# Optimization experiments

Hardware: AMD Instinct MI355X
Metric: run time of the kernel (lower is better)

The kernel has to match this reference:

```python
import jax, jax.numpy as jnp
import numpy as np

N = 10000
E = 320000
IN_CH = 256
OUT4 = 256  # 4 * out_channels, out_channels = 64


def setup_inputs() -> dict:
    key = jax.random.key(0)
    k1, k2, k3 = jax.random.split(key, 3)
    x = jax.random.normal(k1, (N, IN_CH), dtype=jnp.float32)
    edge_index = jax.random.randint(k2, (2, E), 0, N, dtype=jnp.int64)
    stdv = 1.0 / np.sqrt(64.0)  # 1/sqrt(out_channels), as in __init__
    weight = jax.random.uniform(k3, (IN_CH, OUT4), dtype=jnp.float32,
                                minval=-stdv, maxval=stdv)
    return {"x": x, "weight": weight, "edge_index": edge_index}


def reference(x, weight, edge_index):
    n = x.shape[0]
    idx = jnp.arange(n)
    # dense adjacency with self-loops (duplicates/edges just set to 1)
    adj = jnp.zeros((n, n), dtype=x.dtype)
    adj = adj.at[idx, idx].set(1.0)
    adj = adj.at[edge_index[0], edge_index[1]].set(1.0)
    # symmetric degree normalization D^-1/2 A D^-1/2
    deg = jnp.sum(adj, axis=1)  # >= 1 due to self-loops
    d_inv_sqrt = jax.lax.rsqrt(deg)
    norm_adj = adj * d_inv_sqrt[:, None] * d_inv_sqrt[None, :]
    # aggregate then project: (A_norm @ x) @ W
    return jnp.matmul(jnp.matmul(norm_adj, x), weight)
```

## Files before the change

kernel.cpp:

```cpp
#include <hip/hip_runtime.h>


#define CH 256
#define ELLW 96
#define FB 80
#define RPB 125

typedef __attribute__((ext_vector_type(8))) short short8;
typedef __attribute__((ext_vector_type(4))) float f32x4;

__device__ inline unsigned short f2b(float f) {
    unsigned x = __builtin_bit_cast(unsigned, f);
    x = (x + 0x7fffu + ((x >> 16) & 1u)) >> 16;
    return (unsigned short)x;
}
__device__ inline float b2f(unsigned short u) {
    unsigned v = ((unsigned)u) << 16;
    return __builtin_bit_cast(float, v);
}

__global__ void prep_kernel(const float* __restrict__ w,
                            unsigned short* __restrict__ wt) {
    int idx = blockIdx.x * blockDim.x + threadIdx.x;
    if (idx < CH * CH) {
        int k = idx >> 8, nn = idx & 255;
        wt[nn * CH + k] = f2b(w[idx]);
    }
}

__global__ __launch_bounds__(1024) void fillgemm_kernel(
    const int* __restrict__ ei, int e_cnt, int* __restrict__ cnt,
    int* __restrict__ col_ell,
    const float* __restrict__ x, const unsigned short* __restrict__ wt,
    unsigned short* __restrict__ zb, int n) {
    __shared__ int lcnt[RPB];
    if ((int)blockIdx.x < FB) {
        const int lo = blockIdx.x * RPB;
        for (int i = threadIdx.x; i < RPB; i += 1024) lcnt[i] = 0;
        __syncthreads();
        const int4* r4 = (const int4*)ei;
        const int4* c4 = (const int4*)(ei + e_cnt);
        const int n4 = e_cnt >> 2;
        for (int i = threadIdx.x; i < n4; i += 1024) {
            int4 rv = r4[i];
            int4 cv = c4[i];
            int d0 = rv.x - lo, d1 = rv.y - lo, d2 = rv.z - lo, d3 = rv.w - lo;
            if ((unsigned)d0 < RPB) {
                int pos = atomicAdd(&lcnt[d0], 1);
                if (pos < ELLW) col_ell[(size_t)rv.x * ELLW + pos] = cv.x;
            }
            if ((unsigned)d1 < RPB) {
                int pos = atomicAdd(&lcnt[d1], 1);
                if (pos < ELLW) col_ell[(size_t)rv.y * ELLW + pos] = cv.y;
            }
            if ((unsigned)d2 < RPB) {
                int pos = atomicAdd(&lcnt[d2], 1);
                if (pos < ELLW) col_ell[(size_t)rv.z * ELLW + pos] = cv.z;
            }
            if ((unsigned)d3 < RPB) {
                int pos = atomicAdd(&lcnt[d3], 1);
                if (pos < ELLW) col_ell[(size_t)rv.w * ELLW + pos] = cv.w;
            }
        }
        __syncthreads();
        for (int i = threadIdx.x; i < RPB; i += 1024) cnt[lo + i] = lcnt[i];
        return;
    }
    const int blk = blockIdx.x - FB;
    const int tid = threadIdx.x;
    const int lane = tid & 63;
    const int wv = tid >> 6;
    const int m0 = blk * 64 + (wv >> 2) * 16;
    if (m0 >= n) return;
    const int n0 = (wv & 3) * 64;
    const int rsel = lane & 15;
    const int kbase = (lane >> 4) * 8;

    const float* xrow = x + (size_t)(m0 + rsel) * CH + kbase;
    const unsigned short* b0p = wt + (size_t)(n0 + rsel) * CH + kbase;
    const unsigned short* b1p = b0p + 16 * CH;
    const unsigned short* b2p = b0p + 32 * CH;
    const unsigned short* b3p = b0p + 48 * CH;

    f32x4 acc0 = {0.f, 0.f, 0.f, 0.f};
    f32x4 acc1 = acc0, acc2 = acc0, acc3 = acc0;

#pragma unroll
    for (int kc = 0; kc < 8; ++kc) {
        const float4* p = (const float4*)(xrow + kc * 32);
        float4 u = p[0], v = p[1];
        short8 a;
        a[0] = (short)f2b(u.x); a[1] = (short)f2b(u.y);
        a[2] = (short)f2b(u.z); a[3] = (short)f2b(u.w);
        a[4] = (short)f2b(v.x); a[5] = (short)f2b(v.y);
        a[6] = (short)f2b(v.z); a[7] = (short)f2b(v.w);
        short8 b0 = *(const short8*)(b0p + kc * 32);
        short8 b1 = *(const short8*)(b1p + kc * 32);
        short8 b2 = *(const short8*)(b2p + kc * 32);
        short8 b3 = *(const short8*)(b3p + kc * 32);
        acc0 = __builtin_amdgcn_mfma_f32_16x16x32_bf16(a, b0, acc0, 0, 0, 0);
        acc1 = __builtin_amdgcn_mfma_f32_16x16x32_bf16(a, b1, acc1, 0, 0, 0);
        acc2 = __builtin_amdgcn_mfma_f32_16x16x32_bf16(a, b2, acc2, 0, 0, 0);
        acc3 = __builtin_amdgcn_mfma_f32_16x16x32_bf16(a, b3, acc3, 0, 0, 0);
    }

    const int r0 = (lane >> 4) * 4;
    const int slice = n0 >> 7;
    const int nn0 = n0 & 127;
#pragma unroll
    for (int j = 0; j < 4; ++j) {
        unsigned short* zr = zb + ((size_t)slice * n + (m0 + r0 + j)) * 128 + nn0 + rsel;
        zr[0]  = f2b(acc0[j]);
        zr[16] = f2b(acc1[j]);
        zr[32] = f2b(acc2[j]);
        zr[48] = f2b(acc3[j]);
    }
}

__global__ __launch_bounds__(256) void dedup_kernel(
    int* cnt, int* __restrict__ col_ell, float* __restrict__ dinv, int n) {
    __shared__ int sh[4][ELLW];
    const int wv = threadIdx.x >> 6, lane = threadIdx.x & 63;
    const int r = blockIdx.x * 4 + wv;

    int m = 0;
    if (r < n) { m = cnt[r]; if (m > ELLW) m = ELLW; }
    for (int e = lane; e < m; e += 64) sh[wv][e] = col_ell[(size_t)r * ELLW + e];
    __syncthreads();

    if (r < n) {
        const int e0 = lane, e1 = 64 + lane;
        int c0 = (e0 < m) ? sh[wv][e0] : -1;
        int c1 = (e1 < m) ? sh[wv][e1] : -1;
        bool dup0 = (c0 == r), dup1 = (c1 == r);
        for (int k = 0; k < m; ++k) {
            int ck = sh[wv][k];
            dup0 |= (k < e0) && (ck == c0);
            dup1 |= (k < e1) && (ck == c1);
        }
        unsigned long long b0 = __ballot((e0 < m) && !dup0);
        unsigned long long b1 = __ballot((e1 < m) && !dup1);
        unsigned long long lt = (1ull << lane) - 1ull;
        int n0 = __popcll(b0);
        int mm = n0 + __popcll(b1);
        if (mm != m) {
            if ((e0 < m) && !dup0)
                col_ell[(size_t)r * ELLW + __popcll(b0 & lt)] = c0;
            if ((e1 < m) && !dup1)
                col_ell[(size_t)r * ELLW + n0 + __popcll(b1 & lt)] = c1;
            if (lane == 0) cnt[r] = mm;
        }
        if (lane == 0) dinv[r] = rsqrtf((float)(mm + 1));
    }
}

__global__ __launch_bounds__(256) void gather_kernel(
    const int* __restrict__ cnt, const int* __restrict__ col_ell,
    const float* __restrict__ dinv,
    const unsigned short* __restrict__ zb, float* __restrict__ out, int n) {
    const int b = blockIdx.x;
    const int slice = b & 1;
    const int wv = threadIdx.x >> 6;
    const int wid = (b >> 1) * 4 + wv;
    if (wid >= n) return;
    const int lane = threadIdx.x & 63;
    const int g = lane >> 4;
    const int chb = (lane & 15) * 8;
    int m = cnt[wid]; if (m > ELLW) m = ELLW;
    const int* cl = col_ell + (size_t)wid * ELLW;
    const unsigned short* zs = zb + (size_t)slice * n * 128 + chb;
    const float dr = dinv[wid];

    float acc[8];
    if (g == 0) {
        short8 s = *(const short8*)(zs + (size_t)wid * 128);
#pragma unroll
        for (int q = 0; q < 8; ++q) acc[q] = dr * b2f((unsigned short)s[q]);
    } else {
#pragma unroll
        for (int q = 0; q < 8; ++q) acc[q] = 0.f;
    }

    int idx = g;
    for (; idx + 12 < m; idx += 16) {
        int c0 = cl[idx], c1 = cl[idx + 4], c2 = cl[idx + 8], c3 = cl[idx + 12];
        float d0 = dinv[c0], d1 = dinv[c1], d2 = dinv[c2], d3 = dinv[c3];
        short8 v0 = *(const short8*)(zs + (size_t)c0 * 128);
        short8 v1 = *(const short8*)(zs + (size_t)c1 * 128);
        short8 v2 = *(const short8*)(zs + (size_t)c2 * 128);
        short8 v3 = *(const short8*)(zs + (size_t)c3 * 128);
#pragma unroll
        for (int q = 0; q < 8; ++q)
            acc[q] += d0 * b2f((unsigned short)v0[q]) + d1 * b2f((unsigned short)v1[q])
                    + d2 * b2f((unsigned short)v2[q]) + d3 * b2f((unsigned short)v3[q]);
    }
    for (; idx < m; idx += 4) {
        int c = cl[idx];
        float dc = dinv[c];
        short8 v = *(const short8*)(zs + (size_t)c * 128);
#pragma unroll
        for (int q = 0; q < 8; ++q) acc[q] += dc * b2f((unsigned short)v[q]);
    }

#pragma unroll
    for (int q = 0; q < 8; ++q) acc[q] += __shfl_xor(acc[q], 16);
#pragma unroll
    for (int q = 0; q < 8; ++q) acc[q] += __shfl_xor(acc[q], 32);

    if (g == 0) {
        float* dst = out + (size_t)wid * CH + slice * 128 + chb;
        float4 o0, o1;
        o0.x = acc[0] * dr; o0.y = acc[1] * dr; o0.z = acc[2] * dr; o0.w = acc[3] * dr;
        o1.x = acc[4] * dr; o1.y = acc[5] * dr; o1.z = acc[6] * dr; o1.w = acc[7] * dr;
        *(float4*)dst = o0;
        *(float4*)(dst + 4) = o1;
    }
}

extern "C" void kernel_launch(void* const* d_in, const int* in_sizes, int n_in,
                              void* d_out, int out_size, void* d_ws, size_t ws_size,
                              hipStream_t stream) {
    const float* x = (const float*)d_in[0];
    const float* w = (const float*)d_in[1];
    const int* ei = (const int*)d_in[2];
    float* out = (float*)d_out;

    const int n = in_sizes[0] / CH;
    const int e_cnt = in_sizes[2] / 2;

    char* ws = (char*)d_ws;
    size_t off = 0;
    unsigned short* zb = (unsigned short*)(ws + off); off += (size_t)n * CH * 2;
    unsigned short* wt = (unsigned short*)(ws + off); off += (size_t)CH * CH * 2;
    int* cnt = (int*)(ws + off);      off += (size_t)n * 4;
    float* dinv = (float*)(ws + off); off += (size_t)n * 4;
    int* col_ell = (int*)(ws + off);  off += (size_t)n * ELLW * 4;

    prep_kernel<<<(CH * CH + 255) / 256, 256, 0, stream>>>(w, wt);

    const int gemmb = (n + 63) / 64;
    fillgemm_kernel<<<FB + gemmb, 1024, 0, stream>>>(ei, e_cnt, cnt, col_ell,
                                                     x, wt, zb, n);

    dedup_kernel<<<(n + 3) / 4, 256, 0, stream>>>(cnt, col_ell, dinv, n);

    gather_kernel<<<2 * ((n + 3) / 4), 256, 0, stream>>>(cnt, col_ell, dinv, zb, out, n);
}
```

Before: 87.21 us.

## Fuse dedup into ELL build using shared-memory staging, shrink block to 512

The edge-fill blocks now stage each row's column list in a shared-memory ELL tile and deduplicate it in place, writing the compacted columns, counts and inverse degree straight to global memory. The separate dedup kernel launch and its global re-read of col_ell are removed. Block size drops from 1024 to 512 threads, so GEMM blocks now cover 32 rows each. The catch is a large static shared allocation (~48KB) that every block reserves, GEMM blocks included, which may cut occupancy. Each fill block also scans all edges with half as many threads.

```diff
diff --git a/kernel.cpp b/kernel.cpp
--- a/kernel.cpp
+++ b/kernel.cpp
@@ -5,6 +5,7 @@
 #define ELLW 96
 #define FB 80
 #define RPB 125
+#define BT 512
 
 typedef __attribute__((ext_vector_type(8))) short short8;
 typedef __attribute__((ext_vector_type(4))) float f32x4;
@@ -28,49 +29,77 @@
     }
 }
 
-__global__ __launch_bounds__(1024) void fillgemm_kernel(
+__global__ __launch_bounds__(BT, 2) void buildgemm_kernel(
     const int* __restrict__ ei, int e_cnt, int* __restrict__ cnt,
-    int* __restrict__ col_ell,
+    int* __restrict__ col_ell, float* __restrict__ dinv,
     const float* __restrict__ x, const unsigned short* __restrict__ wt,
     unsigned short* __restrict__ zb, int n) {
+    __shared__ int lcol[RPB][ELLW];
     __shared__ int lcnt[RPB];
     if ((int)blockIdx.x < FB) {
         const int lo = blockIdx.x * RPB;
-        for (int i = threadIdx.x; i < RPB; i += 1024) lcnt[i] = 0;
+        for (int i = threadIdx.x; i < RPB; i += BT) lcnt[i] = 0;
         __syncthreads();
         const int4* r4 = (const int4*)ei;
         const int4* c4 = (const int4*)(ei + e_cnt);
         const int n4 = e_cnt >> 2;
-        for (int i = threadIdx.x; i < n4; i += 1024) {
+        for (int i = threadIdx.x; i < n4; i += BT) {
             int4 rv = r4[i];
             int4 cv = c4[i];
             int d0 = rv.x - lo, d1 = rv.y - lo, d2 = rv.z - lo, d3 = rv.w - lo;
             if ((unsigned)d0 < RPB) {
                 int pos = atomicAdd(&lcnt[d0], 1);
-                if (pos < ELLW) col_ell[(size_t)rv.x * ELLW + pos] = cv.x;
+                if (pos < ELLW) lcol[d0][pos] = cv.x;
             }
             if ((unsigned)d1 < RPB) {
                 int pos = atomicAdd(&lcnt[d1], 1);
-                if (pos < ELLW) col_ell[(size_t)rv.y * ELLW + pos] = cv.y;
+                if (pos < ELLW) lcol[d1][pos] = cv.y;
             }
             if ((unsigned)d2 < RPB) {
                 int pos = atomicAdd(&lcnt[d2], 1);
-                if (pos < ELLW) col_ell[(size_t)rv.z * ELLW + pos] = cv.z;
+                if (pos < ELLW) lcol[d2][pos] = cv.z;
             }
             if ((unsigned)d3 < RPB) {
                 int pos = atomicAdd(&lcnt[d3], 1);
-                if (pos < ELLW) col_ell[(size_t)rv.w * ELLW + pos] = cv.w;
+                if (pos < ELLW) lcol[d3][pos] = cv.w;
             }
         }
         __syncthreads();
-        for (int i = threadIdx.x; i < RPB; i += 1024) cnt[lo + i] = lcnt[i];
+        const int wv = threadIdx.x >> 6, lane = threadIdx.x & 63;
+        const unsigned long long lt = (1ull << lane) - 1ull;
+        for (int ri = wv; ri < RPB; ri += BT / 64) {
+            const int r = lo + ri;
+            if (r >= n) break;
+            int m = lcnt[ri]; if (m > ELLW) m = ELLW;
+            const int e0 = lane, e1 = 64 + lane;
+            int c0 = (e0 < m) ? lcol[ri][e0] : -1;
+            int c1 = (e1 < m) ? lcol[ri][e1] : -1;
+            bool dup0 = (c0 == r), dup1 = (c1 == r);
+            for (int k = 0; k < m; ++k) {
+                int ck = lcol[ri][k];
+                dup0 |= (k < e0) && (ck == c0);
+                dup1 |= (k < e1) && (ck == c1);
+            }
+            unsigned long long b0 = __ballot((e0 < m) && !dup0);
+            unsigned long long b1 = __ballot((e1 < m) && !dup1);
+            int n0 = __popcll(b0);
+            int mm = n0 + __popcll(b1);
+            if ((e0 < m) && !dup0)
+                col_ell[(size_t)r * ELLW + __popcll(b0 & lt)] = c0;
+            if ((e1 < m) && !dup1)
+                col_ell[(size_t)r * ELLW + n0 + __popcll(b1 & lt)] = c1;
+            if (lane == 0) {
+                cnt[r] = mm;
+                dinv[r] = rsqrtf((float)(mm + 1));
+            }
+        }
         return;
     }
     const int blk = blockIdx.x - FB;
     const int tid = threadIdx.x;
     const int lane = tid & 63;
     const int wv = tid >> 6;
-    const int m0 = blk * 64 + (wv >> 2) * 16;
+    const int m0 = blk * 32 + (wv >> 2) * 16;
     if (m0 >= n) return;
     const int n0 = (wv & 3) * 64;
     const int rsel = lane & 15;
@@ -117,43 +146,6 @@
     }
 }
 
-__global__ __launch_bounds__(256) void dedup_kernel(
-    int* cnt, int* __restrict__ col_ell, float* __restrict__ dinv, int n) {
-    __shared__ int sh[4][ELLW];
-    const int wv = threadIdx.x >> 6, lane = threadIdx.x & 63;
-    const int r = blockIdx.x * 4 + wv;
-
-    int m = 0;
-    if (r < n) { m = cnt[r]; if (m > ELLW) m = ELLW; }
-    for (int e = lane; e < m; e += 64) sh[wv][e] = col_ell[(size_t)r * ELLW + e];
-    __syncthreads();
-
-    if (r < n) {
-        const int e0 = lane, e1 = 64 + lane;
-        int c0 = (e0 < m) ? sh[wv][e0] : -1;
-        int c1 = (e1 < m) ? sh[wv][e1] : -1;
-        bool dup0 = (c0 == r), dup1 = (c1 == r);
-        for (int k = 0; k < m; ++k) {
-            int ck = sh[wv][k];
-            dup0 |= (k < e0) && (ck == c0);
-            dup1 |= (k < e1) && (ck == c1);
-        }
-        unsigned long long b0 = __ballot((e0 < m) && !dup0);
-        unsigned long long b1 = __ballot((e1 < m) && !dup1);
-        unsigned long long lt = (1ull << lane) - 1ull;
-        int n0 = __popcll(b0);
-        int mm = n0 + __popcll(b1);
-        if (mm != m) {
-            if ((e0 < m) && !dup0)
-                col_ell[(size_t)r * ELLW + __popcll(b0 & lt)] = c0;
-            if ((e1 < m) && !dup1)
-                col_ell[(size_t)r * ELLW + n0 + __popcll(b1 & lt)] = c1;
-            if (lane == 0) cnt[r] = mm;
-        }
-        if (lane == 0) dinv[r] = rsqrtf((float)(mm + 1));
-    }
-}
-
 __global__ __launch_bounds__(256) void gather_kernel(
     const int* __restrict__ cnt, const int* __restrict__ col_ell,
     const float* __restrict__ dinv,
@@ -238,11 +230,9 @@
 
     prep_kernel<<<(CH * CH + 255) / 256, 256, 0, stream>>>(w, wt);
 
-    const int gemmb = (n + 63) / 64;
-    fillgemm_kernel<<<FB + gemmb, 1024, 0, stream>>>(ei, e_cnt, cnt, col_ell,
-                                                     x, wt, zb, n);
-
-    dedup_kernel<<<(n + 3) / 4, 256, 0, stream>>>(cnt, col_ell, dinv, n);
+    const int gemmb = (n + 31) / 32;
+    buildgemm_kernel<<<FB + gemmb, BT, 0, stream>>>(ei, e_cnt, cnt, col_ell, dinv,
+                                                    x, wt, zb, n);
 
     gather_kernel<<<2 * ((n + 3) / 4), 256, 0, stream>>>(cnt, col_ell, dinv, zb, out, n);
 }
```

After: 136.0 us. 55.9% more time.
